# Optimization experiments

Hardware: AMD Instinct MI355X
Metric: run time of the kernel (lower is better)

## Reference

```python
import jax, jax.numpy as jnp
import numpy as np
import math

HIDDEN = 4096
N_HEADS = 32
N_KV_HEADS = 8
HEAD_DIM = HIDDEN // N_HEADS  # 128
N_GROUPS = N_HEADS // N_KV_HEADS  # 4
ROPE_THETA = 10000.0


def setup_inputs() -> dict:
    key = jax.random.key(0)
    ks = jax.random.split(key, 5)
    B, S = 2, 2048
    hidden_states = jax.random.normal(ks[0], (B, S, HIDDEN), dtype=jnp.float32)
    position_ids = jnp.broadcast_to(jnp.arange(S, dtype=jnp.int32)[None, :], (B, S))
    sc = 1.0 / math.sqrt(HIDDEN)
    Wq = jax.random.normal(ks[1], (HIDDEN, N_HEADS * HEAD_DIM), dtype=jnp.float32) * sc
    Wk = jax.random.normal(ks[2], (HIDDEN, N_KV_HEADS * HEAD_DIM), dtype=jnp.float32) * sc
    Wv = jax.random.normal(ks[3], (HIDDEN, N_KV_HEADS * HEAD_DIM), dtype=jnp.float32) * sc
    Wo = jax.random.normal(ks[4], (HIDDEN, HIDDEN), dtype=jnp.float32) * sc
    return {"hidden_states": hidden_states, "position_ids": position_ids,
            "Wq": Wq, "Wk": Wk, "Wv": Wv, "Wo": Wo}


def _rope_cos_sin(position_ids):
    # inv_freq: [head_dim//2]
    inv_freq = 1.0 / (ROPE_THETA ** (jnp.arange(0, HEAD_DIM, 2, dtype=jnp.float32) / HEAD_DIM))
    freqs = position_ids.astype(jnp.float32)[..., None] * inv_freq  # [B, S, hd/2]
    emb = jnp.concatenate([freqs, freqs], axis=-1)  # [B, S, hd]
    return jnp.cos(emb), jnp.sin(emb)


def _rotate_half(x):
    h = x.shape[-1] // 2
    return jnp.concatenate([-x[..., h:], x[..., :h]], axis=-1)


def _apply_rope(x, cos, sin):
    # x: [B, H, S, hd]; cos/sin: [B, S, hd] -> unsqueeze head dim
    return x * cos[:, None] + _rotate_half(x) * sin[:, None]


def reference(hidden_states, position_ids, Wq, Wk, Wv, Wo):
    B, S, _ = hidden_states.shape
    q = (hidden_states @ Wq).reshape(B, S, N_HEADS, HEAD_DIM).transpose(0, 2, 1, 3)
    k = (hidden_states @ Wk).reshape(B, S, N_KV_HEADS, HEAD_DIM).transpose(0, 2, 1, 3)
    v = (hidden_states @ Wv).reshape(B, S, N_KV_HEADS, HEAD_DIM).transpose(0, 2, 1, 3)

    cos, sin = _rope_cos_sin(position_ids)
    q = _apply_rope(q, cos, sin)
    k = _apply_rope(k, cos, sin)

    # repeat_kv: (B, kvH, S, d) -> (B, H, S, d)
    k = jnp.repeat(k, N_GROUPS, axis=1)
    v = jnp.repeat(v, N_GROUPS, axis=1)

    scores = jnp.einsum('bhqd,bhkd->bhqk', q, k) / math.sqrt(HEAD_DIM)
    causal = jnp.tril(jnp.ones((S, S), dtype=bool))
    neg = jnp.finfo(jnp.float32).min
    scores = jnp.where(causal[None, None], scores, neg)
    attn = jax.nn.softmax(scores.astype(jnp.float32), axis=-1).astype(q.dtype)

    out = jnp.einsum('bhqk,bhkd->bhqd', attn, v)
    out = out.transpose(0, 2, 1, 3).reshape(B, S, HIDDEN)
    return out @ Wo
```

## Files before the change

### kernel.cpp

```cpp
#include <hip/hip_runtime.h>
#include <hip/hip_bf16.h>
#include <math.h>

#define HIDDEN 4096
#define NH 32
#define NKV 8
#define HD 128
#define S_LEN 2048
#define BATCH 2
#define MROWS (BATCH * S_LEN)
#define QKVW 6144

typedef __attribute__((ext_vector_type(8))) __bf16 bf16x8;
typedef __attribute__((ext_vector_type(4))) float f32x4;

__device__ __forceinline__ f32x4 mfma16(bf16x8 a, bf16x8 b, f32x4 c) {
  return __builtin_amdgcn_mfma_f32_16x16x32_bf16(a, b, c, 0, 0, 0);
}

__device__ __forceinline__ void gload16(const __bf16* g, const __bf16* l) {
  __builtin_amdgcn_global_load_lds(
      (const __attribute__((address_space(1))) void*)g,
      (__attribute__((address_space(3))) void*)l, 16, 0, 0);
}

#define SBAR()                          \
  do {                                  \
    __builtin_amdgcn_sched_barrier(0);  \
    __builtin_amdgcn_s_barrier();       \
    __builtin_amdgcn_sched_barrier(0);  \
  } while (0)

__global__ __launch_bounds__(256) void cvt_kernel(const float* __restrict__ in,
                                                  __bf16* __restrict__ out, int n) {
  int i = (blockIdx.x * 256 + threadIdx.x) * 8;
  if (i >= n) return;
  float4 a = *reinterpret_cast<const float4*>(in + i);
  float4 b = *reinterpret_cast<const float4*>(in + i + 4);
  bf16x8 t;
  t[0] = (__bf16)a.x; t[1] = (__bf16)a.y; t[2] = (__bf16)a.z; t[3] = (__bf16)a.w;
  t[4] = (__bf16)b.x; t[5] = (__bf16)b.y; t[6] = (__bf16)b.z; t[7] = (__bf16)b.w;
  *reinterpret_cast<bf16x8*>(out + i) = t;
}

__global__ __launch_bounds__(256) void tcvt_f32(const float* __restrict__ in,
                                                __bf16* __restrict__ out,
                                                int R, int C) {
  __shared__ float t[32][33];
  int tx = threadIdx.x, ty = threadIdx.y;
  int r0 = blockIdx.y * 32, c0 = blockIdx.x * 32;
#pragma unroll
  for (int i = 0; i < 4; i++)
    t[ty + i * 8][tx] = in[(size_t)(r0 + ty + i * 8) * C + c0 + tx];
  __syncthreads();
#pragma unroll
  for (int i = 0; i < 4; i++)
    out[(size_t)(c0 + ty + i * 8) * R + r0 + tx] = (__bf16)t[tx][ty + i * 8];
}

__global__ __launch_bounds__(256) void tvt_kernel(const __bf16* __restrict__ qkv,
                                                  __bf16* __restrict__ vt) {
  __shared__ __bf16 t[32][33];
  int tx = threadIdx.x, ty = threadIdx.y;
  int z = blockIdx.z;
  int b = z >> 3, kvh = z & 7;
  int kv0 = blockIdx.y * 32, d0 = blockIdx.x * 32;
#pragma unroll
  for (int i = 0; i < 4; i++)
    t[ty + i * 8][tx] =
        qkv[(size_t)(b * S_LEN + kv0 + ty + i * 8) * QKVW + 5120 + kvh * HD + d0 + tx];
  __syncthreads();
#pragma unroll
  for (int i = 0; i < 4; i++)
    vt[((size_t)z * HD + d0 + ty + i * 8) * S_LEN + kv0 + tx] = t[tx][ty + i * 8];
}

template<typename CT>
__global__ __launch_bounds__(512, 2) void gemm256(const __bf16* __restrict__ A,
                                                  const __bf16* __restrict__ Bt,
                                                  CT* __restrict__ C,
                                                  int M, int N, int K, int nbx) {
  __shared__ char lds[131072];
  const int tid = threadIdx.x;
  const int l = tid & 63, w = tid >> 6;
  const int lrow = l & 15, lg = l >> 4;
  const int sw = (lrow & 7) << 4;

  int nwg = gridDim.x;
  int swz = (blockIdx.x & 7) * (nwg >> 3) + (blockIdx.x >> 3);
  int bx = swz % nbx, by = swz / nbx;
  int m0 = by * 256, n0 = bx * 256;

  const int rA = w * 8 + (l >> 3);
  const int csw = ((l & 7) ^ (l >> 3)) * 8;
  const __bf16* As_[2][2];
  const __bf16* Bs_[2][2];
#pragma unroll
  for (int h = 0; h < 2; h++)
#pragma unroll
    for (int p = 0; p < 2; p++) {
      As_[h][p] = A + (size_t)(m0 + h * 128 + p * 64 + rA) * K + csw;
      Bs_[h][p] = Bt + (size_t)(n0 + h * 128 + p * 64 + rA) * K + csw;
    }

  auto stageA = [&](int par, int h, int kt) {
#pragma unroll
    for (int p = 0; p < 2; p++)
      gload16(As_[h][p] + kt * 64,
              (const __bf16*)(lds + par * 32768 + h * 16384 + p * 8192 + w * 1024));
  };
  auto stageB = [&](int par, int h, int kt) {
#pragma unroll
    for (int p = 0; p < 2; p++)
      gload16(Bs_[h][p] + kt * 64,
              (const __bf16*)(lds + 65536 + par * 32768 + h * 16384 + p * 8192 + w * 1024));
  };

  const int arbase = (w >> 2) * 64 + lrow;
  const int brbase = (w & 3) * 32 + lrow;

  bf16x8 aA[4][2];
  bf16x8 bB[2][2][2];

  auto readA = [&](int par, int ah) {
#pragma unroll
    for (int i = 0; i < 4; i++)
#pragma unroll
      for (int kk = 0; kk < 2; kk++)
        aA[i][kk] = *reinterpret_cast<const bf16x8*>(
            lds + par * 32768 + (arbase + i * 16 + ah * 128) * 128 +
            ((kk * 64 + lg * 16) ^ sw));
  };
  auto readB = [&](int par, int bh) {
#pragma unroll
    for (int j = 0; j < 2; j++)
#pragma unroll
      for (int kk = 0; kk < 2; kk++)
        bB[bh][j][kk] = *reinterpret_cast<const bf16x8*>(
            lds + 65536 + par * 32768 + (brbase + j * 16 + bh * 128) * 128 +
            ((kk * 64 + lg * 16) ^ sw));
  };

  f32x4 acc[8][4];
#pragma unroll
  for (int i = 0; i < 8; i++)
#pragma unroll
    for (int j = 0; j < 4; j++) {
      acc[i][j][0] = 0.f; acc[i][j][1] = 0.f; acc[i][j][2] = 0.f; acc[i][j][3] = 0.f;
    }

  const int NT = K >> 6;

  stageA(0, 0, 0); stageA(0, 1, 0); stageB(0, 0, 0); stageB(0, 1, 0);
  stageA(1, 0, 1); stageB(1, 0, 1);
  __builtin_amdgcn_sched_barrier(0);
  asm volatile("s_waitcnt vmcnt(4)" ::: "memory");
  SBAR();

  for (int t = 0; t < NT; t++) {
    const int par = t & 1, npar = par ^ 1;
    const int t1 = (t + 1 < NT) ? t + 1 : 0;
    const int t2 = (t + 2 < NT) ? t + 2 : 0;

#define MFMA_QUAD(AH, BH)                                                   \
  __builtin_amdgcn_s_setprio(1);                                            \
  _Pragma("unroll") for (int i4 = 0; i4 < 4; i4++)                          \
      _Pragma("unroll") for (int j2 = 0; j2 < 2; j2++)                      \
          _Pragma("unroll") for (int kk = 0; kk < 2; kk++)                  \
              acc[(AH)*4 + i4][(BH)*2 + j2] =                               \
                  mfma16(aA[i4][kk], bB[BH][j2][kk], acc[(AH)*4 + i4][(BH)*2 + j2]); \
  __builtin_amdgcn_s_setprio(0);

    readA(par, 0);
    readB(par, 0);
    stageA(npar, 1, t1);
    SBAR();
    MFMA_QUAD(0, 0);
    SBAR();
    readB(par, 1);
    stageB(npar, 1, t1);
    SBAR();
    MFMA_QUAD(0, 1);
    SBAR();
    readA(par, 1);
    stageA(par, 0, t2);
    SBAR();
    MFMA_QUAD(1, 0);
    SBAR();
    stageB(par, 0, t2);
    SBAR();
    MFMA_QUAD(1, 1);
    __builtin_amdgcn_sched_barrier(0);
    asm volatile("s_waitcnt vmcnt(4)" ::: "memory");
    SBAR();
#undef MFMA_QUAD
  }

#pragma unroll
  for (int i = 0; i < 8; i++) {
    int row = m0 + (w >> 2) * 64 + (i & 3) * 16 + (i >> 2) * 128 + lg * 4;
#pragma unroll
    for (int j = 0; j < 4; j++) {
      int col = n0 + (w & 3) * 32 + (j & 1) * 16 + (j >> 1) * 128 + lrow;
#pragma unroll
      for (int jj = 0; jj < 4; jj++)
        C[(size_t)(row + jj) * N + col] = (CT)acc[i][j][jj];
    }
  }
}

template<typename CT>
__global__ __launch_bounds__(512, 2) void gemm128(const __bf16* __restrict__ A,
                                                  const __bf16* __restrict__ Bt,
                                                  CT* __restrict__ C,
                                                  int M, int N, int K, int nbx) {
  __shared__ char lds[98304];
  const int tid = threadIdx.x;
  const int l = tid & 63, w = tid >> 6;
  const int lrow = l & 15, lg = l >> 4;
  const int sw = (lrow & 7) << 4;

  int nwg = gridDim.x;
  int swz = (blockIdx.x & 7) * (nwg >> 3) + (blockIdx.x >> 3);
  int bx = swz % nbx, by = swz / nbx;
  int m0 = by * 256, n0 = bx * 128;

  const int rA = w * 8 + (l >> 3);
  const int csw = ((l & 7) ^ (l >> 3)) * 8;
  const __bf16* As_[2][2];
  const __bf16* Bs_[2];
#pragma unroll
  for (int h = 0; h < 2; h++)
#pragma unroll
    for (int p = 0; p < 2; p++)
      As_[h][p] = A + (size_t)(m0 + h * 128 + p * 64 + rA) * K + csw;
#pragma unroll
  for (int p = 0; p < 2; p++)
    Bs_[p] = Bt + (size_t)(n0 + p * 64 + rA) * K + csw;

  auto stageA = [&](int par, int h, int kt) {
#pragma unroll
    for (int p = 0; p < 2; p++)
      gload16(As_[h][p] + kt * 64,
              (const __bf16*)(lds + par * 32768 + h * 16384 + p * 8192 + w * 1024));
  };
  auto stageB = [&](int par, int kt) {
#pragma unroll
    for (int p = 0; p < 2; p++)
      gload16(Bs_[p] + kt * 64,
              (const __bf16*)(lds + 65536 + par * 16384 + p * 8192 + w * 1024));
  };

  const int arbase = (w >> 2) * 64 + lrow;
  const int brbase = (w & 3) * 32 + lrow;

  bf16x8 aA[4][2];
  bf16x8 bB[2][2];

  auto readA = [&](int par, int ah) {
#pragma unroll
    for (int i = 0; i < 4; i++)
#pragma unroll
      for (int kk = 0; kk < 2; kk++)
        aA[i][kk] = *reinterpret_cast<const bf16x8*>(
            lds + par * 32768 + (arbase + i * 16 + ah * 128) * 128 +
            ((kk * 64 + lg * 16) ^ sw));
  };
  auto readB = [&](int par) {
#pragma unroll
    for (int j = 0; j < 2; j++)
#pragma unroll
      for (int kk = 0; kk < 2; kk++)
        bB[j][kk] = *reinterpret_cast<const bf16x8*>(
            lds + 65536 + par * 16384 + (brbase + j * 16) * 128 +
            ((kk * 64 + lg * 16) ^ sw));
  };

  f32x4 acc[8][2];
#pragma unroll
  for (int i = 0; i < 8; i++)
#pragma unroll
    for (int j = 0; j < 2; j++) {
      acc[i][j][0] = 0.f; acc[i][j][1] = 0.f; acc[i][j][2] = 0.f; acc[i][j][3] = 0.f;
    }

  const int NT = K >> 6;

  stageA(0, 0, 0); stageA(0, 1, 0); stageB(0, 0);
  stageA(1, 0, 1);
  __builtin_amdgcn_sched_barrier(0);
  asm volatile("s_waitcnt vmcnt(2)" ::: "memory");
  SBAR();

  for (int t = 0; t < NT; t++) {
    const int par = t & 1, npar = par ^ 1;
    const int t1 = (t + 1 < NT) ? t + 1 : 0;
    const int t2 = (t + 2 < NT) ? t + 2 : 0;

#define MFMA_HALF(AH)                                                        \
  __builtin_amdgcn_s_setprio(1);                                             \
  _Pragma("unroll") for (int i4 = 0; i4 < 4; i4++)                           \
      _Pragma("unroll") for (int j2 = 0; j2 < 2; j2++)                       \
          _Pragma("unroll") for (int kk = 0; kk < 2; kk++)                   \
              acc[(AH)*4 + i4][j2] =                                         \
                  mfma16(aA[i4][kk], bB[j2][kk], acc[(AH)*4 + i4][j2]);      \
  __builtin_amdgcn_s_setprio(0);

    readA(par, 0);
    readB(par);
    stageA(npar, 1, t1);
    stageB(npar, t1);
    SBAR();
    MFMA_HALF(0);
    SBAR();
    readA(par, 1);
    stageA(par, 0, t2);
    SBAR();
    MFMA_HALF(1);
    __builtin_amdgcn_sched_barrier(0);
    asm volatile("s_waitcnt vmcnt(2)" ::: "memory");
    SBAR();
#undef MFMA_HALF
  }

#pragma unroll
  for (int i = 0; i < 8; i++) {
    int row = m0 + (w >> 2) * 64 + (i & 3) * 16 + (i >> 2) * 128 + lg * 4;
#pragma unroll
    for (int j = 0; j < 2; j++) {
      int col = n0 + (w & 3) * 32 + j * 16 + lrow;
#pragma unroll
      for (int jj = 0; jj < 4; jj++)
        C[(size_t)(row + jj) * N + col] = (CT)acc[i][j][jj];
    }
  }
}

__global__ __launch_bounds__(256) void rope_kernel(__bf16* __restrict__ qkv,
                                                   const int* __restrict__ pos) {
  int row = blockIdx.x;
  int t = threadIdx.x;
  float p = (float)pos[row];
  __bf16* rbase = qkv + (size_t)row * QKVW;

  {
    int head = t >> 3, chunk = t & 7;
    __bf16* base = rbase + head * HD + chunk * 8;
    bf16x8 x1 = *reinterpret_cast<const bf16x8*>(base);
    bf16x8 x2 = *reinterpret_cast<const bf16x8*>(base + 64);
    bf16x8 o1, o2;
#pragma unroll
    for (int e = 0; e < 8; e++) {
      float ang = p * exp2f(-0.20762050f * (float)(chunk * 8 + e));
      float s, c;
      __sincosf(ang, &s, &c);
      float a = (float)x1[e], b2 = (float)x2[e];
      o1[e] = (__bf16)(a * c - b2 * s);
      o2[e] = (__bf16)(b2 * c + a * s);
    }
    *reinterpret_cast<bf16x8*>(base) = o1;
    *reinterpret_cast<bf16x8*>(base + 64) = o2;
  }
  if (t < 64) {
    int head = t >> 3, chunk = t & 7;
    __bf16* base = rbase + 4096 + head * HD + chunk * 8;
    bf16x8 x1 = *reinterpret_cast<const bf16x8*>(base);
    bf16x8 x2 = *reinterpret_cast<const bf16x8*>(base + 64);
    bf16x8 o1, o2;
#pragma unroll
    for (int e = 0; e < 8; e++) {
      float ang = p * exp2f(-0.20762050f * (float)(chunk * 8 + e));
      float s, c;
      __sincosf(ang, &s, &c);
      float a = (float)x1[e], b2 = (float)x2[e];
      o1[e] = (__bf16)(a * c - b2 * s);
      o2[e] = (__bf16)(b2 * c + a * s);
    }
    *reinterpret_cast<bf16x8*>(base) = o1;
    *reinterpret_cast<bf16x8*>(base + 64) = o2;
  }
}

__global__ __launch_bounds__(512) void attn_kernel(const __bf16* __restrict__ qkv,
                                                   const __bf16* __restrict__ vt,
                                                   __bf16* __restrict__ out) {
  __shared__ __bf16 Ks[64 * 128];
  __shared__ __bf16 Vs[128 * 64];
  __shared__ __bf16 Ps[8][32][68];

  int tid = threadIdx.x;
  int l = tid & 63, w = tid >> 6;
  int bid = blockIdx.x;
  int qblk = 7 - (bid >> 6);
  int rem = bid & 63;
  int h = rem & 31, b = rem >> 5;
  int kvh = h >> 2;
  int q0w = qblk * 256 + w * 32;
  int lrow = l & 15, lg = l >> 4;
  int sw = (lrow & 7) << 4;
  const float SCL = 0.08838834764831845f * 1.4426950408889634f;

  const __bf16* kbase = qkv + (size_t)(b * S_LEN) * QKVW + 4096 + kvh * HD;
  const __bf16* vbase = vt + ((size_t)(b * NKV + kvh) * HD) * S_LEN;

  int krow = tid >> 3;
  int kslot = (tid & 7) * 2;
  int vrow = tid >> 2;
  int vslot = (tid & 3) * 2;
  char* KsB = (char*)Ks;
  char* VsB = (char*)Vs;
  int koff0 = krow * 256 + ((kslot * 16) ^ ((krow & 7) << 4));
  int koff1 = krow * 256 + (((kslot + 1) * 16) ^ ((krow & 7) << 4));
  int voff0 = vrow * 128 + ((vslot * 16) ^ ((vrow & 7) << 4));
  int voff1 = vrow * 128 + (((vslot + 1) * 16) ^ ((vrow & 7) << 4));
  const __bf16* kg = kbase + (size_t)krow * QKVW + kslot * 8;
  const __bf16* vg = vbase + (size_t)vrow * S_LEN + vslot * 8;

  bf16x8 qf[2][4];
#pragma unroll
  for (int mi = 0; mi < 2; mi++) {
    const __bf16* qp = qkv + (size_t)(b * S_LEN + q0w + mi * 16 + lrow) * QKVW + h * HD + lg * 8;
#pragma unroll
    for (int kk = 0; kk < 4; kk++) {
      bf16x8 t = *reinterpret_cast<const bf16x8*>(qp + kk * 32);
#pragma unroll
      for (int e = 0; e < 8; e++) t[e] = (__bf16)((float)t[e] * SCL);
      qf[mi][kk] = t;
    }
  }

  f32x4 ov[2][8];
#pragma unroll
  for (int mi = 0; mi < 2; mi++)
#pragma unroll
    for (int n = 0; n < 8; n++) {
      ov[mi][n][0] = 0.f; ov[mi][n][1] = 0.f; ov[mi][n][2] = 0.f; ov[mi][n][3] = 0.f;
    }
  float m[2][4], ssum[2][4];
#pragma unroll
  for (int mi = 0; mi < 2; mi++)
#pragma unroll
    for (int jj = 0; jj < 4; jj++) { m[mi][jj] = -3.0e38f; ssum[mi][jj] = 0.f; }

  int nt = 4 * qblk + 4;
  bf16x8 kr0, kr1, vr0, vr1;

  kr0 = *reinterpret_cast<const bf16x8*>(kg);
  kr1 = *reinterpret_cast<const bf16x8*>(kg + 8);
  vr0 = *reinterpret_cast<const bf16x8*>(vg);
  vr1 = *reinterpret_cast<const bf16x8*>(vg + 8);
  *reinterpret_cast<bf16x8*>(KsB + koff0) = kr0;
  *reinterpret_cast<bf16x8*>(KsB + koff1) = kr1;
  *reinterpret_cast<bf16x8*>(VsB + voff0) = vr0;
  *reinterpret_cast<bf16x8*>(VsB + voff1) = vr1;
  __syncthreads();

  for (int t = 0;; t++) {
    int kv0 = t * 64;
    bool more = (t + 1 < nt);
    if (more) {
      int kvn = kv0 + 64;
      kr0 = *reinterpret_cast<const bf16x8*>(kg + (size_t)kvn * QKVW);
      kr1 = *reinterpret_cast<const bf16x8*>(kg + (size_t)kvn * QKVW + 8);
      vr0 = *reinterpret_cast<const bf16x8*>(vg + kvn);
      vr1 = *reinterpret_cast<const bf16x8*>(vg + kvn + 8);
    }

    bool active = (kv0 <= q0w + 31);
    if (active) {
      f32x4 sc[2][4];
#pragma unroll
      for (int mi = 0; mi < 2; mi++)
#pragma unroll
        for (int c = 0; c < 4; c++) {
          sc[mi][c][0] = 0.f; sc[mi][c][1] = 0.f; sc[mi][c][2] = 0.f; sc[mi][c][3] = 0.f;
        }
#pragma unroll
      for (int c = 0; c < 4; c++) {
        int rb = (c * 16 + lrow) * 256;
#pragma unroll
        for (int kk = 0; kk < 4; kk++) {
          bf16x8 kf = *reinterpret_cast<const bf16x8*>(KsB + rb + ((kk * 64 + lg * 16) ^ sw));
          sc[0][c] = mfma16(qf[0][kk], kf, sc[0][c]);
          sc[1][c] = mfma16(qf[1][kk], kf, sc[1][c]);
        }
      }

      bool bound = (kv0 + 64 > q0w);
      float es[2][4];
      bool anyr = false;
#pragma unroll
      for (int mi = 0; mi < 2; mi++)
#pragma unroll
        for (int jj = 0; jj < 4; jj++) {
          int qidx = q0w + mi * 16 + lg * 4 + jj;
          float s0 = sc[mi][0][jj], s1 = sc[mi][1][jj];
          float s2 = sc[mi][2][jj], s3 = sc[mi][3][jj];
          if (bound) {
            if (kv0 + lrow > qidx)      s0 = -3.0e38f;
            if (kv0 + 16 + lrow > qidx) s1 = -3.0e38f;
            if (kv0 + 32 + lrow > qidx) s2 = -3.0e38f;
            if (kv0 + 48 + lrow > qidx) s3 = -3.0e38f;
          }
          float r = fmaxf(fmaxf(s0, s1), fmaxf(s2, s3));
          r = fmaxf(r, __shfl_xor(r, 1));
          r = fmaxf(r, __shfl_xor(r, 2));
          r = fmaxf(r, __shfl_xor(r, 4));
          r = fmaxf(r, __shfl_xor(r, 8));
          float mo = m[mi][jj];
          float mn = fmaxf(mo, r);
          float e = exp2f(mo - mn);
          es[mi][jj] = e;
          anyr |= (mn > mo);
          m[mi][jj] = mn;
          float p0 = exp2f(s0 - mn), p1 = exp2f(s1 - mn);
          float p2 = exp2f(s2 - mn), p3 = exp2f(s3 - mn);
          ssum[mi][jj] = ssum[mi][jj] * e + ((p0 + p1) + (p2 + p3));
          int pr = mi * 16 + lg * 4 + jj;
          Ps[w][pr][lrow]      = (__bf16)p0;
          Ps[w][pr][16 + lrow] = (__bf16)p1;
          Ps[w][pr][32 + lrow] = (__bf16)p2;
          Ps[w][pr][48 + lrow] = (__bf16)p3;
        }
      if (__any(anyr)) {
#pragma unroll
        for (int mi = 0; mi < 2; mi++)
#pragma unroll
          for (int n = 0; n < 8; n++)
#pragma unroll
            for (int jj = 0; jj < 4; jj++) ov[mi][n][jj] *= es[mi][jj];
      }

#pragma unroll
      for (int kvs = 0; kvs < 2; kvs++) {
        bf16x8 pf0 = *reinterpret_cast<const bf16x8*>(&Ps[w][lrow][kvs * 32 + lg * 8]);
        bf16x8 pf1 = *reinterpret_cast<const bf16x8*>(&Ps[w][16 + lrow][kvs * 32 + lg * 8]);
#pragma unroll
        for (int n = 0; n < 8; n++) {
          bf16x8 vf = *reinterpret_cast<const bf16x8*>(
              VsB + (n * 16 + lrow) * 128 + ((kvs * 64 + lg * 16) ^ sw));
          ov[0][n] = mfma16(pf0, vf, ov[0][n]);
          ov[1][n] = mfma16(pf1, vf, ov[1][n]);
        }
      }
    }

    if (!more) break;
    __syncthreads();
    *reinterpret_cast<bf16x8*>(KsB + koff0) = kr0;
    *reinterpret_cast<bf16x8*>(KsB + koff1) = kr1;
    *reinterpret_cast<bf16x8*>(VsB + voff0) = vr0;
    *reinterpret_cast<bf16x8*>(VsB + voff1) = vr1;
    __syncthreads();
  }

  float rinv[2][4];
#pragma unroll
  for (int mi = 0; mi < 2; mi++)
#pragma unroll
    for (int jj = 0; jj < 4; jj++) {
      float s = ssum[mi][jj];
      s += __shfl_xor(s, 1);
      s += __shfl_xor(s, 2);
      s += __shfl_xor(s, 4);
      s += __shfl_xor(s, 8);
      rinv[mi][jj] = 1.0f / s;
    }
#pragma unroll
  for (int mi = 0; mi < 2; mi++)
#pragma unroll
    for (int n = 0; n < 8; n++)
#pragma unroll
      for (int jj = 0; jj < 4; jj++) {
        out[(size_t)(b * S_LEN + q0w + mi * 16 + lg * 4 + jj) * HIDDEN + h * HD + n * 16 + lrow] =
            (__bf16)(ov[mi][n][jj] * rinv[mi][jj]);
      }
}

extern "C" void kernel_launch(void* const* d_in, const int* in_sizes, int n_in,
                              void* d_out, int out_size, void* d_ws, size_t ws_size,
                              hipStream_t stream) {
  const float* hidden = (const float*)d_in[0];
  const int* posids   = (const int*)d_in[1];
  const float* Wq     = (const float*)d_in[2];
  const float* Wk     = (const float*)d_in[3];
  const float* Wv     = (const float*)d_in[4];
  const float* Wo     = (const float*)d_in[5];
  float* out = (float*)d_out;

  char* ws = (char*)d_ws;
  __bf16* h_bf    = (__bf16*)(ws + 0);
  __bf16* a_buf   = h_bf;
  __bf16* Wt      = (__bf16*)(ws + 33554432);
  __bf16* qkv_buf = (__bf16*)(ws + 83886080);
  __bf16* vt_buf  = (__bf16*)(ws + 134217728);

  dim3 b256(256), b328(32, 8), b512(512);

  cvt_kernel<<<dim3(MROWS * HIDDEN / (256 * 8)), b256, 0, stream>>>(hidden, h_bf, MROWS * HIDDEN);

  tcvt_f32<<<dim3(HIDDEN / 32, HIDDEN / 32), b328, 0, stream>>>(Wq, Wt, HIDDEN, HIDDEN);
  tcvt_f32<<<dim3((NKV * HD) / 32, HIDDEN / 32), b328, 0, stream>>>(
      Wk, Wt + (size_t)4096 * 4096, HIDDEN, NKV * HD);
  tcvt_f32<<<dim3((NKV * HD) / 32, HIDDEN / 32), b328, 0, stream>>>(
      Wv, Wt + (size_t)5120 * 4096, HIDDEN, NKV * HD);

  gemm128<__bf16><<<dim3((QKVW / 128) * (MROWS / 256)), b512, 0, stream>>>(
      h_bf, Wt, qkv_buf, MROWS, QKVW, HIDDEN, QKVW / 128);

  rope_kernel<<<dim3(MROWS), b256, 0, stream>>>(qkv_buf, posids);

  tvt_kernel<<<dim3(HD / 32, S_LEN / 32, BATCH * NKV), b328, 0, stream>>>(qkv_buf, vt_buf);

  attn_kernel<<<dim3(8 * NH * BATCH), b512, 0, stream>>>(qkv_buf, vt_buf, a_buf);

  tcvt_f32<<<dim3(HIDDEN / 32, HIDDEN / 32), b328, 0, stream>>>(Wo, Wt, HIDDEN, HIDDEN);

  gemm256<float><<<dim3((HIDDEN / 256) * (MROWS / 256)), b512, 0, stream>>>(
      a_buf, Wt, out, MROWS, HIDDEN, HIDDEN, HIDDEN / 256);
}
```

Before: 555.8 us.

## Split QKV GEMM into 256/128 tiles, fuse weight transposes, lazy softmax rescale

Merges the three Wq/Wk/Wv transpose-convert launches into one 3D-grid kernel. The QKV projection becomes a 256-wide-tile GEMM for the Q columns plus a 128-wide-tile GEMM for the K/V columns, so fewer B tiles are reloaded. Attention now orders the second half of its query blocks ascending for load balance and raises wave priority around the MFMA sections. It also skips rescaling the output unless the running max grows by more than 8 in log2 units, which allows unnormalized values up to 2^8 in bf16 P and risks some accuracy.

```diff
diff --git a/kernel.cpp b/kernel.cpp
--- a/kernel.cpp
+++ b/kernel.cpp
@@ -43,6 +43,30 @@
   *reinterpret_cast<bf16x8*>(out + i) = t;
 }
 
+__global__ __launch_bounds__(256) void tcvt3_kernel(const float* __restrict__ Wq,
+                                                    const float* __restrict__ Wk,
+                                                    const float* __restrict__ Wv,
+                                                    __bf16* __restrict__ Wt) {
+  __shared__ float t[32][33];
+  int z = blockIdx.z;
+  const float* in;
+  __bf16* out;
+  int C;
+  if (z == 0)      { in = Wq; out = Wt;                         C = 4096; }
+  else if (z == 1) { in = Wk; out = Wt + (size_t)4096 * 4096;   C = 1024; }
+  else             { in = Wv; out = Wt + (size_t)5120 * 4096;   C = 1024; }
+  if ((int)blockIdx.x * 32 >= C) return;
+  int tx = threadIdx.x, ty = threadIdx.y;
+  int r0 = blockIdx.y * 32, c0 = blockIdx.x * 32;
+#pragma unroll
+  for (int i = 0; i < 4; i++)
+    t[ty + i * 8][tx] = in[(size_t)(r0 + ty + i * 8) * C + c0 + tx];
+  __syncthreads();
+#pragma unroll
+  for (int i = 0; i < 4; i++)
+    out[(size_t)(c0 + ty + i * 8) * 4096 + r0 + tx] = (__bf16)t[tx][ty + i * 8];
+}
+
 __global__ __launch_bounds__(256) void tcvt_f32(const float* __restrict__ in,
                                                 __bf16* __restrict__ out,
                                                 int R, int C) {
@@ -79,7 +103,7 @@
 __global__ __launch_bounds__(512, 2) void gemm256(const __bf16* __restrict__ A,
                                                   const __bf16* __restrict__ Bt,
                                                   CT* __restrict__ C,
-                                                  int M, int N, int K, int nbx) {
+                                                  int K, int ldc, int nbx) {
   __shared__ char lds[131072];
   const int tid = threadIdx.x;
   const int l = tid & 63, w = tid >> 6;
@@ -204,7 +228,7 @@
       int col = n0 + (w & 3) * 32 + (j & 1) * 16 + (j >> 1) * 128 + lrow;
 #pragma unroll
       for (int jj = 0; jj < 4; jj++)
-        C[(size_t)(row + jj) * N + col] = (CT)acc[i][j][jj];
+        C[(size_t)(row + jj) * ldc + col] = (CT)acc[i][j][jj];
     }
   }
 }
@@ -213,7 +237,7 @@
 __global__ __launch_bounds__(512, 2) void gemm128(const __bf16* __restrict__ A,
                                                   const __bf16* __restrict__ Bt,
                                                   CT* __restrict__ C,
-                                                  int M, int N, int K, int nbx) {
+                                                  int K, int ldc, int nbx) {
   __shared__ char lds[98304];
   const int tid = threadIdx.x;
   const int l = tid & 63, w = tid >> 6;
@@ -331,7 +355,7 @@
       int col = n0 + (w & 3) * 32 + j * 16 + lrow;
 #pragma unroll
       for (int jj = 0; jj < 4; jj++)
-        C[(size_t)(row + jj) * N + col] = (CT)acc[i][j][jj];
+        C[(size_t)(row + jj) * ldc + col] = (CT)acc[i][j][jj];
     }
   }
 }
@@ -391,7 +415,7 @@
   int tid = threadIdx.x;
   int l = tid & 63, w = tid >> 6;
   int bid = blockIdx.x;
-  int qblk = 7 - (bid >> 6);
+  int qblk = (bid < 256) ? (7 - (bid >> 6)) : ((bid - 256) >> 6);
   int rem = bid & 63;
   int h = rem & 31, b = rem >> 5;
   int kvh = h >> 2;
@@ -475,6 +499,7 @@
         for (int c = 0; c < 4; c++) {
           sc[mi][c][0] = 0.f; sc[mi][c][1] = 0.f; sc[mi][c][2] = 0.f; sc[mi][c][3] = 0.f;
         }
+      __builtin_amdgcn_s_setprio(1);
 #pragma unroll
       for (int c = 0; c < 4; c++) {
         int rb = (c * 16 + lrow) * 256;
@@ -485,6 +510,7 @@
           sc[1][c] = mfma16(qf[1][kk], kf, sc[1][c]);
         }
       }
+      __builtin_amdgcn_s_setprio(0);
 
       bool bound = (kv0 + 64 > q0w);
       float es[2][4];
@@ -508,10 +534,11 @@
           r = fmaxf(r, __shfl_xor(r, 4));
           r = fmaxf(r, __shfl_xor(r, 8));
           float mo = m[mi][jj];
-          float mn = fmaxf(mo, r);
-          float e = exp2f(mo - mn);
+          bool grow = (r > mo + 8.0f);
+          float mn = grow ? r : mo;
+          float e = grow ? exp2f(mo - r) : 1.0f;
           es[mi][jj] = e;
-          anyr |= (mn > mo);
+          anyr |= grow;
           m[mi][jj] = mn;
           float p0 = exp2f(s0 - mn), p1 = exp2f(s1 - mn);
           float p2 = exp2f(s2 - mn), p3 = exp2f(s3 - mn);
@@ -531,6 +558,7 @@
             for (int jj = 0; jj < 4; jj++) ov[mi][n][jj] *= es[mi][jj];
       }
 
+      __builtin_amdgcn_s_setprio(1);
 #pragma unroll
       for (int kvs = 0; kvs < 2; kvs++) {
         bf16x8 pf0 = *reinterpret_cast<const bf16x8*>(&Ps[w][lrow][kvs * 32 + lg * 8]);
@@ -543,6 +571,7 @@
           ov[1][n] = mfma16(pf1, vf, ov[1][n]);
         }
       }
+      __builtin_amdgcn_s_setprio(0);
     }
 
     if (!more) break;
@@ -599,14 +628,12 @@
 
   cvt_kernel<<<dim3(MROWS * HIDDEN / (256 * 8)), b256, 0, stream>>>(hidden, h_bf, MROWS * HIDDEN);
 
-  tcvt_f32<<<dim3(HIDDEN / 32, HIDDEN / 32), b328, 0, stream>>>(Wq, Wt, HIDDEN, HIDDEN);
-  tcvt_f32<<<dim3((NKV * HD) / 32, HIDDEN / 32), b328, 0, stream>>>(
-      Wk, Wt + (size_t)4096 * 4096, HIDDEN, NKV * HD);
-  tcvt_f32<<<dim3((NKV * HD) / 32, HIDDEN / 32), b328, 0, stream>>>(
-      Wv, Wt + (size_t)5120 * 4096, HIDDEN, NKV * HD);
-
-  gemm128<__bf16><<<dim3((QKVW / 128) * (MROWS / 256)), b512, 0, stream>>>(
-      h_bf, Wt, qkv_buf, MROWS, QKVW, HIDDEN, QKVW / 128);
+  tcvt3_kernel<<<dim3(128, 128, 3), b328, 0, stream>>>(Wq, Wk, Wv, Wt);
+
+  gemm256<__bf16><<<dim3(256), b512, 0, stream>>>(
+      h_bf, Wt, qkv_buf, HIDDEN, QKVW, 4096 / 256);
+  gemm128<__bf16><<<dim3(256), b512, 0, stream>>>(
+      h_bf, Wt + (size_t)4096 * 4096, qkv_buf + 4096, HIDDEN, QKVW, 2048 / 128);
 
   rope_kernel<<<dim3(MROWS), b256, 0, stream>>>(qkv_buf, posids);
 
@@ -616,6 +643,6 @@
 
   tcvt_f32<<<dim3(HIDDEN / 32, HIDDEN / 32), b328, 0, stream>>>(Wo, Wt, HIDDEN, HIDDEN);
 
-  gemm256<float><<<dim3((HIDDEN / 256) * (MROWS / 256)), b512, 0, stream>>>(
-      a_buf, Wt, out, MROWS, HIDDEN, HIDDEN, HIDDEN / 256);
-}
+  gemm256<float><<<dim3(256), b512, 0, stream>>>(
+      a_buf, Wt, out, HIDDEN, HIDDEN, HIDDEN / 256);
+}
```

Measured after the change: 564.6 us. Within noise of the previous version (+1.6%).
